# Kernel optimization log

Hardware: AMD Instinct MI355X
Metric: run time of the kernel (lower is better)

Reference implementation:

```python
import jax, jax.numpy as jnp
import numpy as np

DIM = 4096
N_HEADS = 32
N_KV_HEADS = 8
HEAD_DIM = DIM // N_HEADS  # 128
N_REP = N_HEADS // N_KV_HEADS  # 4
FFN_HIDDEN = 11008
EPS = 1e-6
B, S = 4, 2048


def rms_norm(x, gamma):
    # x: [b, s, d]
    var = jnp.mean(x * x, axis=-1, keepdims=True)
    return gamma * (x * jax.lax.rsqrt(var + EPS))


def apply_rope(x, cos, sin):
    # x: [b, s, h, d]; cos/sin: [s, d/2]. Complex rotation on (even, odd) pairs.
    x2 = x.reshape(*x.shape[:-1], HEAD_DIM // 2, 2)
    x0, x1 = x2[..., 0], x2[..., 1]
    c = cos[None, :, None, :]
    s = sin[None, :, None, :]
    r0 = x0 * c - x1 * s
    r1 = x0 * s + x1 * c
    return jnp.stack([r0, r1], axis=-1).reshape(x.shape)


def setup_inputs() -> dict:
    key = jax.random.key(0)
    ks = jax.random.split(key, 16)
    sc = 0.02
    inp = {
        "x": jax.random.normal(ks[0], (B, S, DIM), dtype=jnp.float32),
        "freqs": jax.random.uniform(ks[1], (S, HEAD_DIM // 2), dtype=jnp.float32) * (2 * np.pi),
        "start_pos": 0,
        "gamma_attn": jnp.ones((DIM,), jnp.float32),
        "gamma_ffn": jnp.ones((DIM,), jnp.float32),
        "wq_w": sc * jax.random.normal(ks[2], (N_HEADS * HEAD_DIM, DIM), jnp.float32),
        "wq_b": jnp.zeros((N_HEADS * HEAD_DIM,), jnp.float32),
        "wk_w": sc * jax.random.normal(ks[3], (N_KV_HEADS * HEAD_DIM, DIM), jnp.float32),
        "wk_b": jnp.zeros((N_KV_HEADS * HEAD_DIM,), jnp.float32),
        "wv_w": sc * jax.random.normal(ks[4], (N_KV_HEADS * HEAD_DIM, DIM), jnp.float32),
        "wv_b": jnp.zeros((N_KV_HEADS * HEAD_DIM,), jnp.float32),
        "wo_w": sc * jax.random.normal(ks[5], (DIM, N_HEADS * HEAD_DIM), jnp.float32),
        "wo_b": jnp.zeros((DIM,), jnp.float32),
        "w1_w": sc * jax.random.normal(ks[6], (FFN_HIDDEN, DIM), jnp.float32),
        "w3_w": sc * jax.random.normal(ks[7], (FFN_HIDDEN, DIM), jnp.float32),
        "w2_w": sc * jax.random.normal(ks[8], (DIM, FFN_HIDDEN), jnp.float32),
    }
    return inp


def reference(x, freqs, start_pos, gamma_attn, gamma_ffn,
              wq_w, wq_b, wk_w, wk_b, wv_w, wv_b, wo_w, wo_b,
              w1_w, w3_w, w2_w):
    cos, sin = jnp.cos(freqs), jnp.sin(freqs)

    # --- attention sublayer ---
    xn = rms_norm(x, gamma_attn)
    xq = (xn @ wq_w.T + wq_b).reshape(B, S, N_HEADS, HEAD_DIM)
    xk = (xn @ wk_w.T + wk_b).reshape(B, S, N_KV_HEADS, HEAD_DIM)
    xv = (xn @ wv_w.T + wv_b).reshape(B, S, N_KV_HEADS, HEAD_DIM)
    xq = apply_rope(xq, cos, sin)
    xk = apply_rope(xk, cos, sin)

    # KV cache: start_pos=0 prefill -> cache slice [0:start_pos+S] == current xk/xv
    keys = jnp.repeat(xk, N_REP, axis=2)   # [b, s, n_heads, d]
    values = jnp.repeat(xv, N_REP, axis=2)

    scores = jnp.einsum('bqhd,bkhd->bhqk', xq, keys) / np.sqrt(HEAD_DIM)
    probs = jax.nn.softmax(scores.astype(jnp.float32), axis=-1).astype(xq.dtype)
    attn = jnp.einsum('bhqk,bkhd->bqhd', probs, values).reshape(B, S, DIM)
    h = x + attn @ wo_w.T + wo_b

    # --- FFN sublayer (LLaMA SwiGLU) ---
    hn = rms_norm(h, gamma_ffn)
    ff = (jax.nn.silu(hn @ w1_w.T) * (hn @ w3_w.T)) @ w2_w.T
    return h + ff
```

## Files before the change

### kernel.cpp

```cpp
#include <hip/hip_runtime.h>
#include <hip/hip_bf16.h>

#define DIM   4096
#define NH    32
#define NKV   8
#define HD    128
#define FFNH  11008
#define BATCH 4
#define SEQ   2048
#define MTOT  (BATCH*SEQ)

using bf16x8_t = __attribute__((ext_vector_type(8))) short;
using f32x4_t  = __attribute__((ext_vector_type(4))) float;

typedef const __attribute__((address_space(1))) unsigned int GlbU32;
typedef __attribute__((address_space(3))) unsigned int LdsU32;

__device__ __forceinline__ unsigned short f2b(float f) {
  union { float f; unsigned int u; } v; v.f = f;
  return (unsigned short)((v.u + 0x7fffu + ((v.u >> 16) & 1u)) >> 16);
}
__device__ __forceinline__ float b2f(unsigned short b) {
  union { unsigned int u; float f; } v; v.u = ((unsigned int)b) << 16;
  return v.f;
}
__device__ __forceinline__ void gll16(const void* g, void* l) {
  __builtin_amdgcn_global_load_lds((GlbU32*)g, (LdsU32*)l, 16, 0, 0);
}

#define VM8  asm volatile("s_waitcnt vmcnt(8)" ::: "memory")
#define VM4M asm volatile("s_waitcnt vmcnt(4)" ::: "memory")
#define VM0  asm volatile("s_waitcnt vmcnt(0)" ::: "memory")

__global__ __launch_bounds__(256)
void cvt_bf16_k(const float* __restrict__ src, unsigned short* __restrict__ dst)
{
  const size_t i = ((size_t)blockIdx.x * 256 + threadIdx.x) * 8;
  const float4 a = *(const float4*)&src[i];
  const float4 b = *(const float4*)&src[i + 4];
  union { int4 v; unsigned short u[8]; } o;
  o.u[0] = f2b(a.x); o.u[1] = f2b(a.y); o.u[2] = f2b(a.z); o.u[3] = f2b(a.w);
  o.u[4] = f2b(b.x); o.u[5] = f2b(b.y); o.u[6] = f2b(b.z); o.u[7] = f2b(b.w);
  *(int4*)&dst[i] = o.v;
}

__global__ __launch_bounds__(256)
void rmsnorm_k(const float* __restrict__ X, const float* __restrict__ gamma,
               unsigned short* __restrict__ Y)
{
  const int row = blockIdx.x, t = threadIdx.x;
  const float* xr = X + (size_t)row * DIM;
  float4 v[4];
  float ss = 0.f;
#pragma unroll
  for (int p = 0; p < 4; ++p) {
    v[p] = *(const float4*)&xr[p * 1024 + t * 4];
    ss += v[p].x*v[p].x + v[p].y*v[p].y + v[p].z*v[p].z + v[p].w*v[p].w;
  }
#pragma unroll
  for (int off = 32; off >= 1; off >>= 1) ss += __shfl_xor(ss, off, 64);
  __shared__ float red[4];
  if ((t & 63) == 0) red[t >> 6] = ss;
  __syncthreads();
  const float tot = red[0] + red[1] + red[2] + red[3];
  const float rn = rsqrtf(tot * (1.f / DIM) + 1e-6f);
  unsigned short* yr = Y + (size_t)row * DIM;
#pragma unroll
  for (int p = 0; p < 4; ++p) {
    const float4 gv = *(const float4*)&gamma[p * 1024 + t * 4];
    short4 o;
    o.x = (short)f2b(v[p].x * gv.x * rn);
    o.y = (short)f2b(v[p].y * gv.y * rn);
    o.z = (short)f2b(v[p].z * gv.z * rn);
    o.w = (short)f2b(v[p].w * gv.w * rn);
    *(short4*)&yr[p * 1024 + t * 4] = o;
  }
}

template<int NHT>
__global__ __launch_bounds__(256)
void rope_k(unsigned short* __restrict__ buf, const float* __restrict__ fr)
{
  const int u = blockIdx.x * 256 + threadIdx.x;
  const int per_row = NHT * 16;
  const int row  = u / per_row;
  const int rem  = u - row * per_row;
  const int head = rem >> 4;
  const int i4   = (rem & 15) << 2;
  const int s    = row & (SEQ - 1);
  unsigned short* p = buf + (size_t)row * (NHT * HD) + head * HD + i4 * 2;
  union { int4 v; unsigned short u16[8]; } d;
  d.v = *(const int4*)p;
  const float4 f = *(const float4*)&fr[s * 64 + i4];
  const float fa[4] = {f.x, f.y, f.z, f.w};
#pragma unroll
  for (int i = 0; i < 4; ++i) {
    float sn, c;
    __sincosf(fa[i], &sn, &c);
    const float x0 = b2f(d.u16[2*i]), x1 = b2f(d.u16[2*i+1]);
    d.u16[2*i]   = f2b(x0 * c - x1 * sn);
    d.u16[2*i+1] = f2b(x0 * sn + x1 * c);
  }
  *(int4*)p = d.v;
}

template<int MODE>
__global__ __launch_bounds__(512)
void gemm256(const unsigned short* __restrict__ A,
             const unsigned short* __restrict__ W,
             const unsigned short* __restrict__ W3p,
             const float* __restrict__ bias,
             const float* res,
             float* outF,
             unsigned short* __restrict__ outH,
             const unsigned short* __restrict__ wkp,
             const unsigned short* __restrict__ wvp,
             const float* __restrict__ bkp,
             const float* __restrict__ bvp,
             unsigned short* __restrict__ okp,
             unsigned short* __restrict__ ovp,
             int K)
{
  __shared__ __align__(16) char smem[131072];
  const int t = threadIdx.x, lane = t & 63, wid = t >> 6;
  const int wr = wid >> 2, wc = wid & 3;
  const int G = gridDim.x, bid = blockIdx.x;
  const int wg = (bid & 7) * (G >> 3) + (bid >> 3);
  const int NBN = G >> 5;
  const int span = NBN << 3;
  const int tmg = wg / span, rr = wg - tmg * span;
  const int tn = rr >> 3, tm = (tmg << 3) + (rr & 7);
  const int m0 = tm << 8;
  const int NSUB = K >> 5;

  const unsigned short *P1, *P2;
  const float* bp = bias;
  unsigned short* oh = outH;
  int nloc = 0, colsN = 4096;
  if constexpr (MODE == 0) {
    const int n0 = tn << 8;
    if (n0 < 4096)      { nloc = n0;        P1 = W   + (size_t)nloc * K; bp = bias; oh = outH; colsN = 4096; }
    else if (n0 < 5120) { nloc = n0 - 4096; P1 = wkp + (size_t)nloc * K; bp = bkp;  oh = okp;  colsN = 1024; }
    else                { nloc = n0 - 5120; P1 = wvp + (size_t)nloc * K; bp = bvp;  oh = ovp;  colsN = 1024; }
    P2 = P1 + (size_t)128 * K;
  } else if constexpr (MODE == 3) {
    const int n0w = tn << 7;
    P1 = W   + (size_t)n0w * K;
    P2 = W3p + (size_t)n0w * K;
    nloc = n0w;
  } else {
    const int n0 = tn << 8;
    P1 = W + (size_t)n0 * K;
    P2 = P1 + (size_t)128 * K;
    nloc = n0;
  }

  const int r0 = t >> 2, gg = t & 3;
  const int gsw = gg ^ ((r0 >> 1) & 3);

  auto stA = [&](int sig) {
    if (sig < NSUB) {
      const int slot = sig & 3;
      gll16(A + (size_t)(m0 + r0) * K + sig * 32 + gsw * 8,
            smem + slot * 16384 + wid * 1024);
      gll16(A + (size_t)(m0 + 128 + r0) * K + sig * 32 + gsw * 8,
            smem + slot * 16384 + 8192 + wid * 1024);
    }
  };
  auto stB = [&](int sig) {
    if (sig < NSUB) {
      const int slot = sig & 3;
      gll16(P1 + (size_t)r0 * K + sig * 32 + gsw * 8,
            smem + 65536 + slot * 16384 + wid * 1024);
      gll16(P2 + (size_t)r0 * K + sig * 32 + gsw * 8,
            smem + 65536 + slot * 16384 + 8192 + wid * 1024);
    }
  };
  auto rdA = [&](int slot, int mo) -> bf16x8_t {
    const int lrow = wr * 128 + mo + (lane & 15);
    const int g = (lane >> 4) ^ ((lrow >> 1) & 3);
    return *(const bf16x8_t*)(smem + slot * 16384 + lrow * 64 + g * 16);
  };
  auto rdB = [&](int slot, int nf) -> bf16x8_t {
    const int brow = wc * 64 + nf * 16 + (lane & 15);
    const int g = (lane >> 4) ^ ((brow >> 1) & 3);
    return *(const bf16x8_t*)(smem + 65536 + slot * 16384 + brow * 64 + g * 16);
  };

  f32x4_t acc[8][4];
#pragma unroll
  for (int i = 0; i < 8; ++i)
#pragma unroll
    for (int j = 0; j < 4; ++j) acc[i][j] = (f32x4_t)0.f;

  stA(0); stB(0); stA(1); stB(1); stA(2); stB(2);
  VM8;
  __builtin_amdgcn_s_barrier();

  for (int p = 0; p < NSUB; ++p) {
    const int slot = p & 3;
    bf16x8_t bfv[4], afv[8];
#pragma unroll
    for (int n = 0; n < 4; ++n) bfv[n] = rdB(slot, n);
#pragma unroll
    for (int m = 0; m < 8; ++m) afv[m] = rdA(slot, m * 16);
    stA(p + 3); stB(p + 3);
    __builtin_amdgcn_s_setprio(1);
#pragma unroll
    for (int m = 0; m < 8; ++m)
#pragma unroll
      for (int n = 0; n < 4; ++n)
        acc[m][n] = __builtin_amdgcn_mfma_f32_16x16x32_bf16(afv[m], bfv[n], acc[m][n], 0, 0, 0);
    __builtin_amdgcn_s_setprio(0);
    if (p < NSUB - 3)      { VM8; }
    else if (p == NSUB - 3){ VM4M; }
    else                   { VM0; }
    __builtin_amdgcn_s_barrier();
  }

  if constexpr (MODE == 0) {
#pragma unroll
    for (int ni = 0; ni < 4; ++ni) {
      const int col = nloc + wc * 64 + ni * 16 + (lane & 15);
      const float bv = bp[col];
#pragma unroll
      for (int mi = 0; mi < 8; ++mi)
#pragma unroll
        for (int r = 0; r < 4; ++r) {
          const int row = m0 + wr * 128 + mi * 16 + (lane >> 4) * 4 + r;
          oh[(size_t)row * colsN + col] = f2b(acc[mi][ni][r] + bv);
        }
    }
  } else if constexpr (MODE == 1 || MODE == 2) {
#pragma unroll
    for (int ni = 0; ni < 4; ++ni) {
      const int col = nloc + wc * 64 + ni * 16 + (lane & 15);
      float bv = 0.f;
      if constexpr (MODE == 1) bv = bias[col];
#pragma unroll
      for (int mi = 0; mi < 8; ++mi)
#pragma unroll
        for (int r = 0; r < 4; ++r) {
          const int row = m0 + wr * 128 + mi * 16 + (lane >> 4) * 4 + r;
          const size_t idx = (size_t)row * 4096 + col;
          outF[idx] = acc[mi][ni][r] + bv + res[idx];
        }
    }
  } else {
    if (wc >= 2) {
      const int widx = wr * 2 + (wc - 2);
#pragma unroll
      for (int ni = 0; ni < 4; ++ni)
#pragma unroll
        for (int mi = 0; mi < 8; ++mi)
#pragma unroll
          for (int r = 0; r < 4; ++r) {
            const int lrow = mi * 16 + (lane >> 4) * 4 + r;
            const int ncol = ni * 16 + (lane & 15);
            *(unsigned short*)(smem + widx * 16384 + lrow * 128 + ncol * 2) =
                f2b(acc[mi][ni][r]);
          }
    }
    __syncthreads();
    if (wc < 2) {
      const int widx = wr * 2 + wc;
#pragma unroll
      for (int ni = 0; ni < 4; ++ni)
#pragma unroll
        for (int mi = 0; mi < 8; ++mi)
#pragma unroll
          for (int r = 0; r < 4; ++r) {
            const int lrow = mi * 16 + (lane >> 4) * 4 + r;
            const int ncol = ni * 16 + (lane & 15);
            const float s3 = b2f(*(const unsigned short*)(smem + widx * 16384 + lrow * 128 + ncol * 2));
            const float s1 = acc[mi][ni][r];
            const float sig = 1.f / (1.f + __expf(-s1));
            const int row = m0 + wr * 128 + lrow;
            outH[(size_t)row * FFNH + nloc + wc * 64 + ncol] = f2b(s1 * sig * s3);
          }
    }
  }
}

__global__ __launch_bounds__(256, 3)
void attn_k(const unsigned short* __restrict__ Q, const unsigned short* __restrict__ Kb,
            const unsigned short* __restrict__ Vb, unsigned short* __restrict__ O)
{
  __shared__ unsigned short Ks[4][4096];
  __shared__ unsigned short Vt[2][4096];
  __shared__ unsigned short Ps[2560];
  const int t = threadIdx.x, lane = t & 63, wid = t >> 6;
  const int bx = blockIdx.x;
  const int qt = bx & 31, h = (bx >> 5) & 31, b = bx >> 10;
  const int kvh = h >> 2;
  const float rs = 0.08838834764831845f;
  constexpr int NPAIR = SEQ / 64;

  const int q0 = wid * 16;
  const int qc = lane & 15;

  bf16x8_t qf[4];
  {
    const unsigned short* qrow = Q + (size_t)(b * SEQ + qt * 64 + q0 + qc) * DIM
                                   + h * HD + (lane >> 4) * 8;
#pragma unroll
    for (int ks = 0; ks < 4; ++ks) qf[ks] = *(const bf16x8_t*)(qrow + ks * 32);
  }

  const unsigned short* Kbase = Kb + (size_t)(b * SEQ) * (NKV * HD) + kvh * HD;
  const unsigned short* Vbase = Vb + (size_t)(b * SEQ) * (NKV * HD) + kvh * HD;

  auto stK = [&](int kt, int slot) {
#pragma unroll
    for (int oo = 0; oo < 2; ++oo) {
      const int o = wid * 2 + oo;
      const int row = o * 4 + (lane >> 4);
      const int gl  = (lane & 15) ^ (row & 7);
      gll16(Kbase + (size_t)(kt * 32 + row) * (NKV * HD) + gl * 8, &Ks[slot][o * 512]);
    }
  };
  const int kv = t >> 3, dc = (t & 7) << 4;
  const int colv = kv ^ ((t & 3) << 3);
  auto ldV = [&](int kt, int4& lo, int4& hi) {
    const unsigned short* gp = Vbase + (size_t)(kt * 32 + kv) * (NKV * HD) + dc;
    lo = *(const int4*)gp;
    hi = *(const int4*)(gp + 8);
  };
  auto wrV = [&](int slot, int4 vlo, int4 vhi) {
    union { int4 v; unsigned short u[8]; } lo, hi;
    lo.v = vlo; hi.v = vhi;
#pragma unroll
    for (int j = 0; j < 8; ++j) Vt[slot][(dc + j) * 32 + colv] = lo.u[j];
#pragma unroll
    for (int j = 0; j < 8; ++j) Vt[slot][(dc + 8 + j) * 32 + colv] = hi.u[j];
  };

  int4 a0l, a0h, a1l, a1h, b0l, b0h, b1l, b1h;
  stK(0, 0); ldV(0, a0l, a0h); stK(1, 1); ldV(1, a1l, a1h);
  stK(2, 2); ldV(2, b0l, b0h); stK(3, 3); ldV(3, b1l, b1h);

  f32x4_t oa[8];
#pragma unroll
  for (int i = 0; i < 8; ++i) oa[i] = (f32x4_t)0.f;
  float mrun = -1e30f, lrun = 0.f;
  const int pbase = wid * 640 + qc * 40;
  const int pwr   = pbase + (lane >> 4) * 4;

  auto pack2 = [&](float x, float y) -> unsigned int {
    return (unsigned int)f2b(x) | ((unsigned int)f2b(y) << 16);
  };

  auto pairIter = [&](int p, int sb, int4& l0, int4& h0, int4& l1, int4& h1) {
    if (p == NPAIR - 1) { VM0; } else { VM8; }
    wrV(0, l0, h0);
    wrV(1, l1, h1);
    asm volatile("s_waitcnt lgkmcnt(0)" ::: "memory");
    __builtin_amdgcn_s_barrier();

    f32x4_t st[4];
    st[0] = (f32x4_t)0.f; st[1] = (f32x4_t)0.f;
    st[2] = (f32x4_t)0.f; st[3] = (f32x4_t)0.f;
    const int kr0 = qc, kr1 = 16 + qc;
    __builtin_amdgcn_s_setprio(1);
#pragma unroll
    for (int ks = 0; ks < 4; ++ks) {
      const bf16x8_t k00 = *(const bf16x8_t*)&Ks[sb][(kr0 * 128 + ks * 32 + (lane >> 4) * 8) ^ ((kr0 & 7) << 3)];
      st[0] = __builtin_amdgcn_mfma_f32_16x16x32_bf16(k00, qf[ks], st[0], 0, 0, 0);
      const bf16x8_t k01 = *(const bf16x8_t*)&Ks[sb][(kr1 * 128 + ks * 32 + (lane >> 4) * 8) ^ ((kr1 & 7) << 3)];
      st[1] = __builtin_amdgcn_mfma_f32_16x16x32_bf16(k01, qf[ks], st[1], 0, 0, 0);
      const bf16x8_t k10 = *(const bf16x8_t*)&Ks[sb + 1][(kr0 * 128 + ks * 32 + (lane >> 4) * 8) ^ ((kr0 & 7) << 3)];
      st[2] = __builtin_amdgcn_mfma_f32_16x16x32_bf16(k10, qf[ks], st[2], 0, 0, 0);
      const bf16x8_t k11 = *(const bf16x8_t*)&Ks[sb + 1][(kr1 * 128 + ks * 32 + (lane >> 4) * 8) ^ ((kr1 & 7) << 3)];
      st[3] = __builtin_amdgcn_mfma_f32_16x16x32_bf16(k11, qf[ks], st[3], 0, 0, 0);
    }
    __builtin_amdgcn_s_setprio(0);

    float mx01 = fmaxf(fmaxf(st[0][0], st[0][1]), fmaxf(st[0][2], st[0][3]));
    float mx23 = fmaxf(fmaxf(st[1][0], st[1][1]), fmaxf(st[1][2], st[1][3]));
    float mx45 = fmaxf(fmaxf(st[2][0], st[2][1]), fmaxf(st[2][2], st[2][3]));
    float mx67 = fmaxf(fmaxf(st[3][0], st[3][1]), fmaxf(st[3][2], st[3][3]));
    float pm = fmaxf(fmaxf(mx01, mx23), fmaxf(mx45, mx67)) * rs;
    pm = fmaxf(pm, __shfl_xor(pm, 16, 64));
    pm = fmaxf(pm, __shfl_xor(pm, 32, 64));

    const int grow = __any(pm > mrun);
    if (grow) {
      const float mnew = fmaxf(mrun, pm);
      const float corr = __expf(mrun - mnew);
      mrun = mnew;
      lrun *= corr;
      float c4[4];
#pragma unroll
      for (int r = 0; r < 4; ++r) c4[r] = __shfl(corr, (lane >> 4) * 4 + r, 16);
#pragma unroll
      for (int i = 0; i < 8; ++i)
#pragma unroll
        for (int r = 0; r < 4; ++r) oa[i][r] *= c4[r];
    }

    float ssum = 0.f;
#pragma unroll
    for (int tt = 0; tt < 4; ++tt)
#pragma unroll
      for (int r = 0; r < 4; ++r) {
        st[tt][r] = __expf(st[tt][r] * rs - mrun);
        ssum += st[tt][r];
      }
    ssum += __shfl_xor(ssum, 16, 64);
    ssum += __shfl_xor(ssum, 32, 64);
    lrun += ssum;

    *(unsigned int*)&Ps[pwr]      = pack2(st[0][0], st[0][1]);
    *(unsigned int*)&Ps[pwr + 2]  = pack2(st[0][2], st[0][3]);
    *(unsigned int*)&Ps[pwr + 16] = pack2(st[1][0], st[1][1]);
    *(unsigned int*)&Ps[pwr + 18] = pack2(st[1][2], st[1][3]);
    const bf16x8_t pa0 = *(const bf16x8_t*)&Ps[pbase + (lane >> 4) * 8];
    asm volatile("s_waitcnt lgkmcnt(0)" ::: "memory");
    *(unsigned int*)&Ps[pwr]      = pack2(st[2][0], st[2][1]);
    *(unsigned int*)&Ps[pwr + 2]  = pack2(st[2][2], st[2][3]);
    *(unsigned int*)&Ps[pwr + 16] = pack2(st[3][0], st[3][1]);
    *(unsigned int*)&Ps[pwr + 18] = pack2(st[3][2], st[3][3]);
    const bf16x8_t pa1 = *(const bf16x8_t*)&Ps[pbase + (lane >> 4) * 8];

    __builtin_amdgcn_s_setprio(1);
#pragma unroll
    for (int nt2 = 0; nt2 < 8; ++nt2) {
      const bf16x8_t vf0 = *(const bf16x8_t*)&Vt[0][(nt2 * 16 + (lane & 15)) * 32 + (((lane >> 4) ^ (nt2 & 3)) << 3)];
      oa[nt2] = __builtin_amdgcn_mfma_f32_16x16x32_bf16(pa0, vf0, oa[nt2], 0, 0, 0);
      const bf16x8_t vf1 = *(const bf16x8_t*)&Vt[1][(nt2 * 16 + (lane & 15)) * 32 + (((lane >> 4) ^ (nt2 & 3)) << 3)];
      oa[nt2] = __builtin_amdgcn_mfma_f32_16x16x32_bf16(pa1, vf1, oa[nt2], 0, 0, 0);
    }
    __builtin_amdgcn_s_setprio(0);
    __builtin_amdgcn_s_barrier();
    if (p + 2 < NPAIR) {
      stK(2 * p + 4, sb);     ldV(2 * p + 4, l0, h0);
      stK(2 * p + 5, sb + 1); ldV(2 * p + 5, l1, h1);
    }
  };

  for (int j = 0; j < NPAIR / 2; ++j) {
    pairIter(2 * j,     0, a0l, a0h, a1l, a1h);
    pairIter(2 * j + 1, 2, b0l, b0h, b1l, b1h);
  }

  float inv[4];
#pragma unroll
  for (int r = 0; r < 4; ++r) inv[r] = 1.f / __shfl(lrun, (lane >> 4) * 4 + r, 16);
#pragma unroll
  for (int nt2 = 0; nt2 < 8; ++nt2) {
    const int col = h * HD + nt2 * 16 + (lane & 15);
#pragma unroll
    for (int r = 0; r < 4; ++r) {
      const int row = qt * 64 + q0 + (lane >> 4) * 4 + r;
      O[(size_t)(b * SEQ + row) * DIM + col] = f2b(oa[nt2][r] * inv[r]);
    }
  }
}

extern "C" void kernel_launch(void* const* d_in, const int* in_sizes, int n_in,
                              void* d_out, int out_size, void* d_ws, size_t ws_size,
                              hipStream_t stream)
{
  (void)in_sizes; (void)n_in; (void)out_size; (void)ws_size;
  const float* x   = (const float*)d_in[0];
  const float* fr  = (const float*)d_in[1];
  const float* ga  = (const float*)d_in[3];
  const float* gf  = (const float*)d_in[4];
  const float* wq  = (const float*)d_in[5];
  const float* wqb = (const float*)d_in[6];
  const float* wk  = (const float*)d_in[7];
  const float* wkb = (const float*)d_in[8];
  const float* wv  = (const float*)d_in[9];
  const float* wvb = (const float*)d_in[10];
  const float* wo  = (const float*)d_in[11];
  const float* wob = (const float*)d_in[12];
  const float* w1  = (const float*)d_in[13];
  const float* w3  = (const float*)d_in[14];
  const float* w2  = (const float*)d_in[15];
  float* out = (float*)d_out;

  constexpr size_t MB = 1ull << 20;
  char* ws = (char*)d_ws;
  unsigned short* xn = (unsigned short*)(ws);
  unsigned short* qb = (unsigned short*)(ws + 64*MB);
  unsigned short* kb = (unsigned short*)(ws + 128*MB);
  unsigned short* vb = (unsigned short*)(ws + 144*MB);
  unsigned short* ao = (unsigned short*)(ws + 160*MB);
  unsigned short* hn = (unsigned short*)(ws + 224*MB);
  unsigned short* g  = (unsigned short*)(ws);
  unsigned short* wscr = (unsigned short*)(ws + 288*MB);
  unsigned short* wqB = wscr;
  unsigned short* wkB = wscr + 16*MB;
  unsigned short* wvB = wscr + 20*MB;
  unsigned short* woB = wscr;
  unsigned short* w1B = wscr;
  unsigned short* w3B = wscr + 45*MB;
  unsigned short* w2B = wscr;

  rmsnorm_k<<<MTOT, 256, 0, stream>>>(x, ga, xn);
  cvt_bf16_k<<<(NH*HD*DIM)/2048,  256, 0, stream>>>(wq, wqB);
  cvt_bf16_k<<<(NKV*HD*DIM)/2048, 256, 0, stream>>>(wk, wkB);
  cvt_bf16_k<<<(NKV*HD*DIM)/2048, 256, 0, stream>>>(wv, wvB);
  gemm256<0><<<(MTOT/256)*((DIM+2*NKV*HD)/256), 512, 0, stream>>>(
      xn, wqB, nullptr, wqb, nullptr, nullptr, qb,
      wkB, wvB, wkb, wvb, kb, vb, DIM);
  rope_k<NH><<<(MTOT*NH*16)/256,  256, 0, stream>>>(qb, fr);
  rope_k<NKV><<<(MTOT*NKV*16)/256,256, 0, stream>>>(kb, fr);
  attn_k<<<BATCH*NH*(SEQ/64), 256, 0, stream>>>(qb, kb, vb, ao);
  cvt_bf16_k<<<(DIM*DIM)/2048, 256, 0, stream>>>(wo, woB);
  gemm256<1><<<(MTOT/256)*(DIM/256), 512, 0, stream>>>(
      ao, woB, nullptr, wob, x, out, nullptr,
      nullptr, nullptr, nullptr, nullptr, nullptr, nullptr, DIM);
  rmsnorm_k<<<MTOT, 256, 0, stream>>>(out, gf, hn);
  cvt_bf16_k<<<(FFNH*DIM)/2048, 256, 0, stream>>>(w1, w1B);
  cvt_bf16_k<<<(FFNH*DIM)/2048, 256, 0, stream>>>(w3, w3B);
  gemm256<3><<<(MTOT/256)*(FFNH/128), 512, 0, stream>>>(
      hn, w1B, w3B, nullptr, nullptr, nullptr, g,
      nullptr, nullptr, nullptr, nullptr, nullptr, nullptr, DIM);
  cvt_bf16_k<<<(FFNH*DIM)/2048, 256, 0, stream>>>(w2, w2B);
  gemm256<2><<<(MTOT/256)*(DIM/256), 512, 0, stream>>>(
      g, w2B, nullptr, nullptr, out, out, nullptr,
      nullptr, nullptr, nullptr, nullptr, nullptr, nullptr, FFNH);
}
```

Measured before the change: 3.631 ms.

## Fuse RoPE into QKV GEMM epilogue and restructure attention V staging

Applies the rotary embedding inside the QKV GEMM epilogue, pairing even and odd columns with a lane shuffle, and removes the two standalone rope kernels and their extra read/write passes over Q and K. The attention kernel now loads 64 keys of V per pair iteration into a single padded transposed LDS tile written as 4-element vectors, and keeps P in two LDS buffers to drop a waitcnt. It also removes the occupancy hint from the attention launch bounds. The epilogue now evaluates sincos per output element, and the changed LDS usage may alter attention occupancy.

```diff
diff --git a/kernel.cpp b/kernel.cpp
--- a/kernel.cpp
+++ b/kernel.cpp
@@ -12,6 +12,7 @@
 
 using bf16x8_t = __attribute__((ext_vector_type(8))) short;
 using f32x4_t  = __attribute__((ext_vector_type(4))) float;
+using u16x4_t  = __attribute__((ext_vector_type(4))) unsigned short;
 
 typedef const __attribute__((address_space(1))) unsigned int GlbU32;
 typedef __attribute__((address_space(3))) unsigned int LdsU32;
@@ -75,33 +76,6 @@
     o.w = (short)f2b(v[p].w * gv.w * rn);
     *(short4*)&yr[p * 1024 + t * 4] = o;
   }
-}
-
-template<int NHT>
-__global__ __launch_bounds__(256)
-void rope_k(unsigned short* __restrict__ buf, const float* __restrict__ fr)
-{
-  const int u = blockIdx.x * 256 + threadIdx.x;
-  const int per_row = NHT * 16;
-  const int row  = u / per_row;
-  const int rem  = u - row * per_row;
-  const int head = rem >> 4;
-  const int i4   = (rem & 15) << 2;
-  const int s    = row & (SEQ - 1);
-  unsigned short* p = buf + (size_t)row * (NHT * HD) + head * HD + i4 * 2;
-  union { int4 v; unsigned short u16[8]; } d;
-  d.v = *(const int4*)p;
-  const float4 f = *(const float4*)&fr[s * 64 + i4];
-  const float fa[4] = {f.x, f.y, f.z, f.w};
-#pragma unroll
-  for (int i = 0; i < 4; ++i) {
-    float sn, c;
-    __sincosf(fa[i], &sn, &c);
-    const float x0 = b2f(d.u16[2*i]), x1 = b2f(d.u16[2*i+1]);
-    d.u16[2*i]   = f2b(x0 * c - x1 * sn);
-    d.u16[2*i+1] = f2b(x0 * sn + x1 * c);
-  }
-  *(int4*)p = d.v;
 }
 
 template<int MODE>
@@ -119,6 +93,7 @@
              const float* __restrict__ bvp,
              unsigned short* __restrict__ okp,
              unsigned short* __restrict__ ovp,
+             const float* __restrict__ freqs,
              int K)
 {
   __shared__ __align__(16) char smem[131072];
@@ -136,11 +111,12 @@
   const unsigned short *P1, *P2;
   const float* bp = bias;
   unsigned short* oh = outH;
+  const float* ropef = nullptr;
   int nloc = 0, colsN = 4096;
   if constexpr (MODE == 0) {
     const int n0 = tn << 8;
-    if (n0 < 4096)      { nloc = n0;        P1 = W   + (size_t)nloc * K; bp = bias; oh = outH; colsN = 4096; }
-    else if (n0 < 5120) { nloc = n0 - 4096; P1 = wkp + (size_t)nloc * K; bp = bkp;  oh = okp;  colsN = 1024; }
+    if (n0 < 4096)      { nloc = n0;        P1 = W   + (size_t)nloc * K; bp = bias; oh = outH; colsN = 4096; ropef = freqs; }
+    else if (n0 < 5120) { nloc = n0 - 4096; P1 = wkp + (size_t)nloc * K; bp = bkp;  oh = okp;  colsN = 1024; ropef = freqs; }
     else                { nloc = n0 - 5120; P1 = wvp + (size_t)nloc * K; bp = bvp;  oh = ovp;  colsN = 1024; }
     P2 = P1 + (size_t)128 * K;
   } else if constexpr (MODE == 3) {
@@ -223,13 +199,23 @@
     for (int ni = 0; ni < 4; ++ni) {
       const int col = nloc + wc * 64 + ni * 16 + (lane & 15);
       const float bv = bp[col];
-#pragma unroll
-      for (int mi = 0; mi < 8; ++mi)
+      const int cin = col & 127;
+#pragma unroll
+      for (int mi = 0; mi < 8; ++mi) {
 #pragma unroll
         for (int r = 0; r < 4; ++r) {
           const int row = m0 + wr * 128 + mi * 16 + (lane >> 4) * 4 + r;
-          oh[(size_t)row * colsN + col] = f2b(acc[mi][ni][r] + bv);
+          float vv = acc[mi][ni][r] + bv;
+          if (ropef) {
+            const float po = __shfl_xor(vv, 1, 64);
+            const float fq = ropef[(row & (SEQ - 1)) * 64 + (cin >> 1)];
+            float sn, cs;
+            __sincosf(fq, &sn, &cs);
+            vv = (col & 1) ? (po * sn + vv * cs) : (vv * cs - po * sn);
+          }
+          oh[(size_t)row * colsN + col] = f2b(vv);
         }
+      }
     }
   } else if constexpr (MODE == 1 || MODE == 2) {
 #pragma unroll
@@ -282,13 +268,13 @@
   }
 }
 
-__global__ __launch_bounds__(256, 3)
+__global__ __launch_bounds__(256)
 void attn_k(const unsigned short* __restrict__ Q, const unsigned short* __restrict__ Kb,
             const unsigned short* __restrict__ Vb, unsigned short* __restrict__ O)
 {
   __shared__ unsigned short Ks[4][4096];
-  __shared__ unsigned short Vt[2][4096];
-  __shared__ unsigned short Ps[2560];
+  __shared__ unsigned short VtU[128 * 68];
+  __shared__ unsigned short Ps[2][2560];
   const int t = threadIdx.x, lane = t & 63, wid = t >> 6;
   const int bx = blockIdx.x;
   const int qt = bx & 31, h = (bx >> 5) & 31, b = bx >> 10;
@@ -319,25 +305,40 @@
       gll16(Kbase + (size_t)(kt * 32 + row) * (NKV * HD) + gl * 8, &Ks[slot][o * 512]);
     }
   };
-  const int kv = t >> 3, dc = (t & 7) << 4;
-  const int colv = kv ^ ((t & 3) << 3);
-  auto ldV = [&](int kt, int4& lo, int4& hi) {
-    const unsigned short* gp = Vbase + (size_t)(kt * 32 + kv) * (NKV * HD) + dc;
-    lo = *(const int4*)gp;
-    hi = *(const int4*)(gp + 8);
-  };
-  auto wrV = [&](int slot, int4 vlo, int4 vhi) {
-    union { int4 v; unsigned short u[8]; } lo, hi;
-    lo.v = vlo; hi.v = vhi;
-#pragma unroll
-    for (int j = 0; j < 8; ++j) Vt[slot][(dc + j) * 32 + colv] = lo.u[j];
-#pragma unroll
-    for (int j = 0; j < 8; ++j) Vt[slot][(dc + 8 + j) * 32 + colv] = hi.u[j];
-  };
-
-  int4 a0l, a0h, a1l, a1h, b0l, b0h, b1l, b1h;
-  stK(0, 0); ldV(0, a0l, a0h); stK(1, 1); ldV(1, a1l, a1h);
-  stK(2, 2); ldV(2, b0l, b0h); stK(3, 3); ldV(3, b1l, b1h);
+
+  const int c8 = t & 15, qq = t >> 4;
+  const int d0 = c8 * 8, kv0 = qq * 4;
+  auto ldV = [&](int kp, int4& w0, int4& w1, int4& w2, int4& w3) {
+    const unsigned short* gp = Vbase + (size_t)(kp * 64 + kv0) * (NKV * HD) + d0;
+    w0 = *(const int4*)gp;
+    w1 = *(const int4*)(gp + NKV * HD);
+    w2 = *(const int4*)(gp + 2 * NKV * HD);
+    w3 = *(const int4*)(gp + 3 * NKV * HD);
+  };
+  auto wrV = [&](int4 w0, int4 w1, int4 w2, int4 w3) {
+    union U { int4 v; unsigned short u[8]; };
+    U a, bb, c, d;
+    a.v = w0; bb.v = w1; c.v = w2; d.v = w3;
+    const int cbase = (qq >> 1) * 8 + (qq & 1) * 4;
+#pragma unroll
+    for (int j = 0; j < 8; ++j) {
+      u16x4_t w = { a.u[j], bb.u[j], c.u[j], d.u[j] };
+      *(u16x4_t*)&VtU[(d0 + j) * 68 + cbase] = w;
+    }
+  };
+  auto rdVf = [&](int tile, int nt2) -> bf16x8_t {
+    const int d = nt2 * 16 + (lane & 15);
+    const int c = (lane >> 4) + tile * 4;
+    const unsigned short* pp = &VtU[d * 68 + c * 8];
+    union { bf16x8_t v; u16x4_t h[2]; } u;
+    u.h[0] = *(const u16x4_t*)pp;
+    u.h[1] = *(const u16x4_t*)(pp + 4);
+    return u.v;
+  };
+
+  int4 a0, a1, a2, a3, b0, b1, b2, b3;
+  stK(0, 0); stK(1, 1); ldV(0, a0, a1, a2, a3);
+  stK(2, 2); stK(3, 3); ldV(1, b0, b1, b2, b3);
 
   f32x4_t oa[8];
 #pragma unroll
@@ -350,10 +351,9 @@
     return (unsigned int)f2b(x) | ((unsigned int)f2b(y) << 16);
   };
 
-  auto pairIter = [&](int p, int sb, int4& l0, int4& h0, int4& l1, int4& h1) {
+  auto pairIter = [&](int p, int sb, int4& w0, int4& w1, int4& w2, int4& w3) {
     if (p == NPAIR - 1) { VM0; } else { VM8; }
-    wrV(0, l0, h0);
-    wrV(1, l1, h1);
+    wrV(w0, w1, w2, w3);
     asm volatile("s_waitcnt lgkmcnt(0)" ::: "memory");
     __builtin_amdgcn_s_barrier();
 
@@ -410,37 +410,36 @@
     ssum += __shfl_xor(ssum, 32, 64);
     lrun += ssum;
 
-    *(unsigned int*)&Ps[pwr]      = pack2(st[0][0], st[0][1]);
-    *(unsigned int*)&Ps[pwr + 2]  = pack2(st[0][2], st[0][3]);
-    *(unsigned int*)&Ps[pwr + 16] = pack2(st[1][0], st[1][1]);
-    *(unsigned int*)&Ps[pwr + 18] = pack2(st[1][2], st[1][3]);
-    const bf16x8_t pa0 = *(const bf16x8_t*)&Ps[pbase + (lane >> 4) * 8];
-    asm volatile("s_waitcnt lgkmcnt(0)" ::: "memory");
-    *(unsigned int*)&Ps[pwr]      = pack2(st[2][0], st[2][1]);
-    *(unsigned int*)&Ps[pwr + 2]  = pack2(st[2][2], st[2][3]);
-    *(unsigned int*)&Ps[pwr + 16] = pack2(st[3][0], st[3][1]);
-    *(unsigned int*)&Ps[pwr + 18] = pack2(st[3][2], st[3][3]);
-    const bf16x8_t pa1 = *(const bf16x8_t*)&Ps[pbase + (lane >> 4) * 8];
+    *(unsigned int*)&Ps[0][pwr]      = pack2(st[0][0], st[0][1]);
+    *(unsigned int*)&Ps[0][pwr + 2]  = pack2(st[0][2], st[0][3]);
+    *(unsigned int*)&Ps[0][pwr + 16] = pack2(st[1][0], st[1][1]);
+    *(unsigned int*)&Ps[0][pwr + 18] = pack2(st[1][2], st[1][3]);
+    *(unsigned int*)&Ps[1][pwr]      = pack2(st[2][0], st[2][1]);
+    *(unsigned int*)&Ps[1][pwr + 2]  = pack2(st[2][2], st[2][3]);
+    *(unsigned int*)&Ps[1][pwr + 16] = pack2(st[3][0], st[3][1]);
+    *(unsigned int*)&Ps[1][pwr + 18] = pack2(st[3][2], st[3][3]);
+    const bf16x8_t pa0 = *(const bf16x8_t*)&Ps[0][pbase + (lane >> 4) * 8];
+    const bf16x8_t pa1 = *(const bf16x8_t*)&Ps[1][pbase + (lane >> 4) * 8];
 
     __builtin_amdgcn_s_setprio(1);
 #pragma unroll
     for (int nt2 = 0; nt2 < 8; ++nt2) {
-      const bf16x8_t vf0 = *(const bf16x8_t*)&Vt[0][(nt2 * 16 + (lane & 15)) * 32 + (((lane >> 4) ^ (nt2 & 3)) << 3)];
+      const bf16x8_t vf0 = rdVf(0, nt2);
       oa[nt2] = __builtin_amdgcn_mfma_f32_16x16x32_bf16(pa0, vf0, oa[nt2], 0, 0, 0);
-      const bf16x8_t vf1 = *(const bf16x8_t*)&Vt[1][(nt2 * 16 + (lane & 15)) * 32 + (((lane >> 4) ^ (nt2 & 3)) << 3)];
+      const bf16x8_t vf1 = rdVf(1, nt2);
       oa[nt2] = __builtin_amdgcn_mfma_f32_16x16x32_bf16(pa1, vf1, oa[nt2], 0, 0, 0);
     }
     __builtin_amdgcn_s_setprio(0);
     __builtin_amdgcn_s_barrier();
     if (p + 2 < NPAIR) {
-      stK(2 * p + 4, sb);     ldV(2 * p + 4, l0, h0);
-      stK(2 * p + 5, sb + 1); ldV(2 * p + 5, l1, h1);
+      stK(2 * p + 4, sb); stK(2 * p + 5, sb + 1);
+      ldV(p + 2, w0, w1, w2, w3);
     }
   };
 
   for (int j = 0; j < NPAIR / 2; ++j) {
-    pairIter(2 * j,     0, a0l, a0h, a1l, a1h);
-    pairIter(2 * j + 1, 2, b0l, b0h, b1l, b1h);
+    pairIter(2 * j,     0, a0, a1, a2, a3);
+    pairIter(2 * j + 1, 2, b0, b1, b2, b3);
   }
 
   float inv[4];
@@ -503,22 +502,20 @@
   cvt_bf16_k<<<(NKV*HD*DIM)/2048, 256, 0, stream>>>(wv, wvB);
   gemm256<0><<<(MTOT/256)*((DIM+2*NKV*HD)/256), 512, 0, stream>>>(
       xn, wqB, nullptr, wqb, nullptr, nullptr, qb,
-      wkB, wvB, wkb, wvb, kb, vb, DIM);
-  rope_k<NH><<<(MTOT*NH*16)/256,  256, 0, stream>>>(qb, fr);
-  rope_k<NKV><<<(MTOT*NKV*16)/256,256, 0, stream>>>(kb, fr);
+      wkB, wvB, wkb, wvb, kb, vb, fr, DIM);
   attn_k<<<BATCH*NH*(SEQ/64), 256, 0, stream>>>(qb, kb, vb, ao);
   cvt_bf16_k<<<(DIM*DIM)/2048, 256, 0, stream>>>(wo, woB);
   gemm256<1><<<(MTOT/256)*(DIM/256), 512, 0, stream>>>(
       ao, woB, nullptr, wob, x, out, nullptr,
-      nullptr, nullptr, nullptr, nullptr, nullptr, nullptr, DIM);
+      nullptr, nullptr, nullptr, nullptr, nullptr, nullptr, nullptr, DIM);
   rmsnorm_k<<<MTOT, 256, 0, stream>>>(out, gf, hn);
   cvt_bf16_k<<<(FFNH*DIM)/2048, 256, 0, stream>>>(w1, w1B);
   cvt_bf16_k<<<(FFNH*DIM)/2048, 256, 0, stream>>>(w3, w3B);
   gemm256<3><<<(MTOT/256)*(FFNH/128), 512, 0, stream>>>(
       hn, w1B, w3B, nullptr, nullptr, nullptr, g,
-      nullptr, nullptr, nullptr, nullptr, nullptr, nullptr, DIM);
+      nullptr, nullptr, nullptr, nullptr, nullptr, nullptr, nullptr, DIM);
   cvt_bf16_k<<<(FFNH*DIM)/2048, 256, 0, stream>>>(w2, w2B);
   gemm256<2><<<(MTOT/256)*(DIM/256), 512, 0, stream>>>(
       g, w2B, nullptr, nullptr, out, out, nullptr,
-      nullptr, nullptr, nullptr, nullptr, nullptr, nullptr, FFNH);
-}
+      nullptr, nullptr, nullptr, nullptr, nullptr, nullptr, nullptr, FFNH);
+}
```

After: 3.797 ms. +4.6%, slower.
